# Kernel tuning notes

Hardware: AMD Instinct MI355X
Metric: run time of the kernel (lower is better)

## Reference

```python
import jax, jax.numpy as jnp
import numpy as np

NUM_HEADS = 32
NUM_KV_HEADS = 8
HEAD_DIM = 128
HIDDEN = 4096
ROPE_THETA = 10000.0
RMS_EPS = 1e-6


def setup_inputs() -> dict:
    key = jax.random.key(0)
    k1, k2, k3 = jax.random.split(key, 3)
    T = 2048
    qkv_out = (NUM_HEADS + 2 * NUM_KV_HEADS) * HEAD_DIM  # 6144
    return {
        "positions": jnp.arange(T, dtype=jnp.int64),
        "hidden_states": jax.random.normal(k1, (T, HIDDEN), dtype=jnp.float32),
        "wqkv": jax.random.normal(k2, (qkv_out, HIDDEN), dtype=jnp.float32) * 0.02,
        "wo": jax.random.normal(k3, (HIDDEN, NUM_HEADS * HEAD_DIM), dtype=jnp.float32) * 0.02,
        "q_norm_w": jnp.ones((HEAD_DIM,), dtype=jnp.float32),
        "k_norm_w": jnp.ones((HEAD_DIM,), dtype=jnp.float32),
    }


def _rms_norm(x, w):
    # per-head RMSNorm over last dim, computed in fp32 (matches Dots1RMSNorm)
    xf = x.astype(jnp.float32)
    var = jnp.mean(xf * xf, axis=-1, keepdims=True)
    return (w * (xf * jax.lax.rsqrt(var + RMS_EPS))).astype(x.dtype)


def _rope(x, positions):
    # NeoX-style rotary: rotate halves. x: [T, H, D]
    half = HEAD_DIM // 2
    inv_freq = 1.0 / (ROPE_THETA ** (jnp.arange(0, half, dtype=jnp.float32) / half))
    ang = positions.astype(jnp.float32)[:, None] * inv_freq  # [T, half]
    cos = jnp.cos(ang)[:, None, :]  # [T,1,half]
    sin = jnp.sin(ang)[:, None, :]
    x1, x2 = x[..., :half], x[..., half:]
    return jnp.concatenate([x1 * cos - x2 * sin, x2 * cos + x1 * sin], axis=-1)


def reference(positions, hidden_states, wqkv, wo, q_norm_w, k_norm_w):
    T = hidden_states.shape[0]
    q_size = NUM_HEADS * HEAD_DIM
    kv_size = NUM_KV_HEADS * HEAD_DIM
    qkv = hidden_states @ wqkv.T  # [T, q_size + 2*kv_size]
    q = qkv[:, :q_size].reshape(T, NUM_HEADS, HEAD_DIM)
    k = qkv[:, q_size:q_size + kv_size].reshape(T, NUM_KV_HEADS, HEAD_DIM)
    v = qkv[:, q_size + kv_size:].reshape(T, NUM_KV_HEADS, HEAD_DIM)

    q = _rms_norm(q, q_norm_w)
    k = _rms_norm(k, k_norm_w)
    q = _rope(q, positions)
    k = _rope(k, positions)

    # GQA: expand kv heads to query heads (group of 4)
    group = NUM_HEADS // NUM_KV_HEADS
    k = jnp.repeat(k, group, axis=1)  # [T, H, D]
    v = jnp.repeat(v, group, axis=1)

    scale = HEAD_DIM ** -0.5
    scores = jnp.einsum('thd,shd->hts', q, k) * scale  # [H, T, T]
    causal = positions[:, None] >= positions[None, :]
    scores = jnp.where(causal[None, :, :], scores, jnp.finfo(scores.dtype).min)
    probs = jax.nn.softmax(scores, axis=-1)
    attn = jnp.einsum('hts,shd->thd', probs, v)  # [T, H, D]
    out = attn.reshape(T, NUM_HEADS * HEAD_DIM) @ wo.T  # [T, HIDDEN]
    return out
```

## Files before the change

kernel.cpp:

```cpp
#include <hip/hip_runtime.h>


#define T_SEQ 2048
#define HID   4096
#define NH    32
#define NKVH  8
#define HD    128
#define QKVN  6144
#define QSZ   4096
#define KVSZ  1024

typedef unsigned short u16;
typedef __attribute__((ext_vector_type(8))) short short8;
typedef __attribute__((ext_vector_type(4))) float floatx4;

__device__ __forceinline__ float bf2f(u16 u) {
  union { unsigned int i; float f; } c; c.i = ((unsigned int)u) << 16; return c.f;
}
__device__ __forceinline__ u16 f2bf(float f) {
  union { float f; unsigned int i; } c; c.f = f;
  unsigned int u = c.i;
  return (u16)((u + 0x7FFFu + ((u >> 16) & 1u)) >> 16);
}
__device__ __forceinline__ floatx4 mfma16(short8 a, short8 b, floatx4 c) {
  return __builtin_amdgcn_mfma_f32_16x16x32_bf16(a, b, c, 0, 0, 0);
}

#define GLD16(g, l) __builtin_amdgcn_global_load_lds( \
    (__attribute__((address_space(1))) unsigned int*)(g), \
    (__attribute__((address_space(3))) unsigned int*)(l), 16, 0, 0)

__global__ __launch_bounds__(256) void cvt_kernel(const float* __restrict__ src,
                                                  u16* __restrict__ dst, int n4) {
  int i = blockIdx.x * 256 + threadIdx.x;
  int stride = gridDim.x * 256;
  for (; i < n4; i += stride) {
    float4 v = ((const float4*)src)[i];
    ushort4 o;
    o.x = f2bf(v.x); o.y = f2bf(v.y); o.z = f2bf(v.z); o.w = f2bf(v.w);
    ((ushort4*)dst)[i] = o;
  }
}

template <int OUT_BF16>
__global__ __launch_bounds__(256, 2) void gemm_bt(const u16* __restrict__ A,
    const u16* __restrict__ B, void* __restrict__ Cv, int M, int N, int K) {
  __shared__ __attribute__((aligned(16))) u16 As[128 * 32];
  __shared__ __attribute__((aligned(16))) u16 Bs[128 * 32];
  const int tid = threadIdx.x;
  const int wave = tid >> 6, lane = tid & 63;
  const int lq = lane >> 4, lc = lane & 15;
  const int wm = wave >> 1, wn = wave & 1;
  const int m0 = blockIdx.y * 128, n0 = blockIdx.x * 128;

  floatx4 acc[4][4];
#pragma unroll
  for (int i = 0; i < 4; ++i)
#pragma unroll
    for (int j = 0; j < 4; ++j) acc[i][j] = {0.f, 0.f, 0.f, 0.f};

  int achunk[4], bchunk[4];
#pragma unroll
  for (int i = 0; i < 4; ++i) {
    int ml = wm * 64 + i * 16 + lc;
    achunk[i] = ml * 4 + (lq ^ ((ml >> 1) & 3));
    int nl = wn * 64 + i * 16 + lc;
    bchunk[i] = nl * 4 + (lq ^ ((nl >> 1) & 3));
  }

  for (int k0 = 0; k0 < K; k0 += 32) {
#pragma unroll
    for (int r = 0; r < 2; ++r) {
      int L = r * 256 + tid;
      int mm = L >> 2;
      int cc = (L & 3) ^ ((mm >> 1) & 3);
      GLD16(A + (size_t)(m0 + mm) * K + k0 + cc * 8,
            As + (size_t)(r * 256 + wave * 64) * 8);
      GLD16(B + (size_t)(n0 + mm) * K + k0 + cc * 8,
            Bs + (size_t)(r * 256 + wave * 64) * 8);
    }
    __syncthreads();
    short8 af[4], bfr[4];
#pragma unroll
    for (int mi = 0; mi < 4; ++mi) af[mi] = *(const short8*)&As[achunk[mi] * 8];
#pragma unroll
    for (int ni = 0; ni < 4; ++ni) bfr[ni] = *(const short8*)&Bs[bchunk[ni] * 8];
#pragma unroll
    for (int mi = 0; mi < 4; ++mi)
#pragma unroll
      for (int ni = 0; ni < 4; ++ni)
        acc[mi][ni] = mfma16(af[mi], bfr[ni], acc[mi][ni]);
    __syncthreads();
  }
#pragma unroll
  for (int mi = 0; mi < 4; ++mi) {
    int row = m0 + wm * 64 + mi * 16 + lq * 4;
#pragma unroll
    for (int ni = 0; ni < 4; ++ni) {
      int col = n0 + wn * 64 + ni * 16 + lc;
#pragma unroll
      for (int r = 0; r < 4; ++r) {
        if (OUT_BF16)
          ((u16*)Cv)[(size_t)(row + r) * N + col] = f2bf(acc[mi][ni][r]);
        else
          ((float*)Cv)[(size_t)(row + r) * N + col] = acc[mi][ni][r];
      }
    }
  }
}

__global__ __launch_bounds__(256) void norm_rope_kernel(const u16* __restrict__ qkv,
    const float* __restrict__ qw, const float* __restrict__ kw,
    u16* __restrict__ Qo, u16* __restrict__ Ko) {
  const int t = blockIdx.x;
  const int hs = blockIdx.y * 4 + (threadIdx.x >> 6);
  const int l = threadIdx.x & 63;
  const bool isq = hs < NH;
  const int col0 = isq ? hs * HD : QSZ + (hs - NH) * HD;
  const u16* src = qkv + (size_t)t * QKVN + col0;
  float x1 = bf2f(src[l]);
  float x2 = bf2f(src[l + 64]);
  float ss = x1 * x1 + x2 * x2;
#pragma unroll
  for (int m = 1; m < 64; m <<= 1) ss += __shfl_xor(ss, m);
  float rstd = rsqrtf(ss * (1.0f / HD) + 1e-6f);
  const float* w = isq ? qw : kw;
  float n1 = x1 * rstd * w[l];
  float n2 = x2 * rstd * w[l + 64];
  float inv = exp2f((float)l * -0.20762050593045158f);
  float ang = (float)t * inv;
  float s, c;
  __sincosf(ang, &s, &c);
  float o1 = n1 * c - n2 * s;
  float o2 = n2 * c + n1 * s;
  if (isq) {
    o1 *= 0.08838834764831845f; o2 *= 0.08838834764831845f;
    u16* dst = Qo + ((size_t)hs * T_SEQ + t) * HD;
    dst[l] = f2bf(o1); dst[l + 64] = f2bf(o2);
  } else {
    u16* dst = Ko + ((size_t)(hs - NH) * T_SEQ + t) * HD;
    dst[l] = f2bf(o1); dst[l + 64] = f2bf(o2);
  }
}

__global__ __launch_bounds__(256) void vtrans_kernel(const u16* __restrict__ qkv,
                                                     u16* __restrict__ VT) {
  __shared__ u16 lds[128][65];
  const int h = blockIdx.y;
  const int t0 = blockIdx.x * 64;
  const int tid = threadIdx.x;
#pragma unroll 4
  for (int i = 0; i < 32; ++i) {
    int f = i * 256 + tid;
    int tl = f >> 7, d = f & 127;
    lds[d][tl] = qkv[(size_t)(t0 + tl) * QKVN + QSZ + KVSZ + h * HD + d];
  }
  __syncthreads();
#pragma unroll 4
  for (int i = 0; i < 32; ++i) {
    int f = i * 256 + tid;
    int d = f >> 6, tl = f & 63;
    VT[((size_t)h * HD + d) * T_SEQ + t0 + tl] = lds[d][tl];
  }
}

__global__ __launch_bounds__(256, 2) void attn_kernel(const u16* __restrict__ Qg,
    const u16* __restrict__ Kg, const u16* __restrict__ VTg, u16* __restrict__ Og) {
  __shared__ __attribute__((aligned(16))) u16 Ks[8192];
  __shared__ __attribute__((aligned(16))) u16 Vs[2][8192];
  __shared__ __attribute__((aligned(16))) u16 Ps[8192];

  const int bid = blockIdx.x;
  const int h = bid & 31;
  const int qq = bid >> 5;
  const int qt = (qq < 8) ? (15 - qq) : (qq - 8);
  const int kvh = h >> 2;
  const int tid = threadIdx.x;
  const int wave = tid >> 6, lane = tid & 63;
  const int lq = lane >> 4, lc = lane & 15;

  const u16* kbase[4];
  const u16* vbase[4];
#pragma unroll
  for (int i = 0; i < 4; ++i) {
    int L = i * 256 + tid;
    int s = L >> 4, cp = L & 15;
    kbase[i] = Kg + ((size_t)kvh * T_SEQ + s) * HD + ((cp ^ (s & 15)) * 8);
    int d = L >> 3, cv = L & 7;
    vbase[i] = VTg + ((size_t)kvh * HD + d) * T_SEQ + ((cv ^ (d & 7)) * 8);
  }

  short8 qf[2][4];
#pragma unroll
  for (int mb = 0; mb < 2; ++mb)
#pragma unroll
    for (int ks = 0; ks < 4; ++ks) {
      int t = qt * 128 + wave * 32 + mb * 16 + lc;
      qf[mb][ks] = *(const short8*)&Qg[((size_t)h * T_SEQ + t) * HD + ks * 32 + lq * 8];
    }

  short8 ones;
#pragma unroll
  for (int j = 0; j < 8; ++j) ones[j] = (short)0x3F80;

  floatx4 of[2][8];
  floatx4 lacc[2];
#pragma unroll
  for (int mb = 0; mb < 2; ++mb) {
    lacc[mb] = {0.f, 0.f, 0.f, 0.f};
#pragma unroll
    for (int db = 0; db < 8; ++db) of[mb][db] = {0.f, 0.f, 0.f, 0.f};
  }

  const int ktmax = 2 * qt + 1;
  const int t0g = qt * 128 + wave * 32;
  const int wave_tmax = t0g + 31;

#pragma unroll
  for (int i = 0; i < 4; ++i) {
    GLD16(kbase[i], Ks + (i * 256 + wave * 64) * 8);
    GLD16(vbase[i], Vs[0] + (i * 256 + wave * 64) * 8);
  }

  for (int kt = 0; kt <= ktmax; ++kt) {
    __syncthreads();
    if (kt + 1 <= ktmax) {
      u16* vd = Vs[(kt + 1) & 1] + (size_t)wave * 64 * 8;
#pragma unroll
      for (int i = 0; i < 4; ++i)
        GLD16(vbase[i] + (kt + 1) * 64, vd + i * 256 * 8);
    }
    const bool active = (kt * 64) <= wave_tmax;
    if (active) {
      floatx4 sf[2][4];
#pragma unroll
      for (int mb = 0; mb < 2; ++mb)
#pragma unroll
        for (int nb = 0; nb < 4; ++nb) sf[mb][nb] = {0.f, 0.f, 0.f, 0.f};
#pragma unroll
      for (int ks = 0; ks < 4; ++ks) {
        short8 kf[4];
#pragma unroll
        for (int nb = 0; nb < 4; ++nb)
          kf[nb] = *(const short8*)&Ks[(nb * 16 + lc) * 128 + ((4 * ks + lq) ^ lc) * 8];
#pragma unroll
        for (int mb = 0; mb < 2; ++mb)
#pragma unroll
          for (int nb = 0; nb < 4; ++nb)
            sf[mb][nb] = mfma16(kf[nb], qf[mb][ks], sf[mb][nb]);
      }
      const bool nm = (kt * 64 + 63) > t0g;
#pragma unroll
      for (int mb = 0; mb < 2; ++mb) {
        const int trow = wave * 32 + mb * 16 + lc;
        const int tg = qt * 128 + trow;
#pragma unroll
        for (int nb = 0; nb < 4; ++nb) {
          ushort4 u;
          float p0 = __expf(sf[mb][nb][0]);
          float p1 = __expf(sf[mb][nb][1]);
          float p2 = __expf(sf[mb][nb][2]);
          float p3 = __expf(sf[mb][nb][3]);
          if (nm) {
            int sg = kt * 64 + nb * 16 + lq * 4;
            p0 = (sg + 0 <= tg) ? p0 : 0.f;
            p1 = (sg + 1 <= tg) ? p1 : 0.f;
            p2 = (sg + 2 <= tg) ? p2 : 0.f;
            p3 = (sg + 3 <= tg) ? p3 : 0.f;
          }
          u.x = f2bf(p0); u.y = f2bf(p1); u.z = f2bf(p2); u.w = f2bf(p3);
          int c = 2 * nb + (lq >> 1);
          *(ushort4*)&Ps[trow * 64 + ((c ^ (trow & 7)) * 8) + (lq & 1) * 4] = u;
        }
      }
    }
    __syncthreads();
    if (kt + 1 <= ktmax) {
      u16* kd = Ks + (size_t)wave * 64 * 8;
#pragma unroll
      for (int i = 0; i < 4; ++i)
        GLD16(kbase[i] + (size_t)(kt + 1) * 8192, kd + i * 256 * 8);
    }
    if (active) {
      const u16* vb = Vs[kt & 1];
      short8 pf[2][2];
#pragma unroll
      for (int mb = 0; mb < 2; ++mb)
#pragma unroll
        for (int k2 = 0; k2 < 2; ++k2) {
          int trow = wave * 32 + mb * 16 + lc;
          pf[mb][k2] =
              *(const short8*)&Ps[trow * 64 + (((4 * k2 + lq) ^ (lc & 7)) * 8)];
        }
#pragma unroll
      for (int k2 = 0; k2 < 2; ++k2) {
#pragma unroll
        for (int db = 0; db < 8; ++db) {
          short8 vf =
              *(const short8*)&vb[(db * 16 + lc) * 64 + (((4 * k2 + lq) ^ (lc & 7)) * 8)];
          of[0][db] = mfma16(pf[0][k2], vf, of[0][db]);
          of[1][db] = mfma16(pf[1][k2], vf, of[1][db]);
        }
        lacc[0] = mfma16(pf[0][k2], ones, lacc[0]);
        lacc[1] = mfma16(pf[1][k2], ones, lacc[1]);
      }
    }
  }
#pragma unroll
  for (int mb = 0; mb < 2; ++mb)
#pragma unroll
    for (int r = 0; r < 4; ++r) {
      float inv = 1.f / lacc[mb][r];
      int tg = qt * 128 + wave * 32 + mb * 16 + lq * 4 + r;
#pragma unroll
      for (int db = 0; db < 8; ++db)
        Og[(size_t)tg * QSZ + h * HD + db * 16 + lc] = f2bf(of[mb][db][r] * inv);
    }
}

extern "C" void kernel_launch(void* const* d_in, const int* in_sizes, int n_in,
                              void* d_out, int out_size, void* d_ws, size_t ws_size,
                              hipStream_t stream) {
  (void)in_sizes; (void)n_in; (void)out_size; (void)ws_size;
  const float* hidden = (const float*)d_in[1];
  const float* wqkv   = (const float*)d_in[2];
  const float* wo     = (const float*)d_in[3];
  const float* qw     = (const float*)d_in[4];
  const float* kw     = (const float*)d_in[5];
  float* out = (float*)d_out;
  char* ws = (char*)d_ws;

  u16* h_bf    = (u16*)(ws + 0);
  u16* wq_bf   = (u16*)(ws + 16777216);
  u16* wo_bf   = (u16*)(ws + 67108864);
  u16* qkv_bf  = (u16*)(ws + 100663296);
  u16* q_bf    = (u16*)(ws + 16777216);
  u16* k_bf    = (u16*)(ws + 33554432);
  u16* vT_bf   = (u16*)(ws + 37748736);
  u16* attn_bf = (u16*)(ws + 0);

  cvt_kernel<<<2048, 256, 0, stream>>>(hidden, h_bf, T_SEQ * HID / 4);
  cvt_kernel<<<4096, 256, 0, stream>>>(wqkv, wq_bf, QKVN * HID / 4);
  cvt_kernel<<<4096, 256, 0, stream>>>(wo, wo_bf, HID * QSZ / 4);

  gemm_bt<1><<<dim3(QKVN / 128, T_SEQ / 128), 256, 0, stream>>>(
      h_bf, wq_bf, qkv_bf, T_SEQ, QKVN, HID);

  norm_rope_kernel<<<dim3(T_SEQ, 10), 256, 0, stream>>>(
      qkv_bf, qw, kw, q_bf, k_bf);
  vtrans_kernel<<<dim3(T_SEQ / 64, NKVH), 256, 0, stream>>>(qkv_bf, vT_bf);

  attn_kernel<<<512, 256, 0, stream>>>(q_bf, k_bf, vT_bf, attn_bf);

  gemm_bt<0><<<dim3(QSZ / 128, T_SEQ / 128), 256, 0, stream>>>(
      attn_bf, wo_bf, out, T_SEQ, QSZ, HID);
}
```

Before: 510.2 us.

## Fuse fp32-to-bf16 conversions, widen GEMM K-tile, and write V transposed from GEMM

The three conversion launches become one kernel that walks all three buffers in a single grid. The GEMM K-tile grows from 32 to 64 with an 8-way XOR swizzle. Blocks are linearized so M tiles vary fastest, which improves reuse of B tiles. The QKV GEMM epilogue writes V columns straight into the transposed VT layout, so the separate transpose kernel and the V part of the intermediate buffer go away. The cost is doubled LDS per block and strided 8-byte stores for the VT output.

```diff
diff --git a/kernel.cpp b/kernel.cpp
--- a/kernel.cpp
+++ b/kernel.cpp
@@ -8,7 +8,7 @@
 #define HD    128
 #define QKVN  6144
 #define QSZ   4096
-#define KVSZ  1024
+#define QKN   5120
 
 typedef unsigned short u16;
 typedef __attribute__((ext_vector_type(8))) short short8;
@@ -30,28 +30,36 @@
     (__attribute__((address_space(1))) unsigned int*)(g), \
     (__attribute__((address_space(3))) unsigned int*)(l), 16, 0, 0)
 
-__global__ __launch_bounds__(256) void cvt_kernel(const float* __restrict__ src,
-                                                  u16* __restrict__ dst, int n4) {
-  int i = blockIdx.x * 256 + threadIdx.x;
+__global__ __launch_bounds__(256) void cvt3_kernel(
+    const float* __restrict__ s0, const float* __restrict__ s1,
+    const float* __restrict__ s2, u16* __restrict__ d0, u16* __restrict__ d1,
+    u16* __restrict__ d2, int n0, int n1, int n2) {
+  int total = n0 + n1 + n2;
   int stride = gridDim.x * 256;
-  for (; i < n4; i += stride) {
-    float4 v = ((const float4*)src)[i];
+  for (int i = blockIdx.x * 256 + threadIdx.x; i < total; i += stride) {
+    const float* s; u16* d; int j = i;
+    if (j < n0)           { s = s0; d = d0; }
+    else if (j < n0 + n1) { j -= n0; s = s1; d = d1; }
+    else                  { j -= n0 + n1; s = s2; d = d2; }
+    float4 v = ((const float4*)s)[j];
     ushort4 o;
     o.x = f2bf(v.x); o.y = f2bf(v.y); o.z = f2bf(v.z); o.w = f2bf(v.w);
-    ((ushort4*)dst)[i] = o;
-  }
-}
-
-template <int OUT_BF16>
+    ((ushort4*)d)[j] = o;
+  }
+}
+
+template <int MODE>
 __global__ __launch_bounds__(256, 2) void gemm_bt(const u16* __restrict__ A,
-    const u16* __restrict__ B, void* __restrict__ Cv, int M, int N, int K) {
-  __shared__ __attribute__((aligned(16))) u16 As[128 * 32];
-  __shared__ __attribute__((aligned(16))) u16 Bs[128 * 32];
+    const u16* __restrict__ B, void* __restrict__ Cv, u16* __restrict__ VT,
+    int mtiles, int K, int ldC) {
+  __shared__ __attribute__((aligned(16))) u16 As[128 * 64];
+  __shared__ __attribute__((aligned(16))) u16 Bs[128 * 64];
   const int tid = threadIdx.x;
   const int wave = tid >> 6, lane = tid & 63;
   const int lq = lane >> 4, lc = lane & 15;
   const int wm = wave >> 1, wn = wave & 1;
-  const int m0 = blockIdx.y * 128, n0 = blockIdx.x * 128;
+  const int by = blockIdx.x % mtiles, bx = blockIdx.x / mtiles;
+  const int m0 = by * 128, n0 = bx * 128;
 
   floatx4 acc[4][4];
 #pragma unroll
@@ -59,57 +67,81 @@
 #pragma unroll
     for (int j = 0; j < 4; ++j) acc[i][j] = {0.f, 0.f, 0.f, 0.f};
 
-  int achunk[4], bchunk[4];
+  int arow[4], brow[4];
 #pragma unroll
   for (int i = 0; i < 4; ++i) {
-    int ml = wm * 64 + i * 16 + lc;
-    achunk[i] = ml * 4 + (lq ^ ((ml >> 1) & 3));
-    int nl = wn * 64 + i * 16 + lc;
-    bchunk[i] = nl * 4 + (lq ^ ((nl >> 1) & 3));
-  }
-
-  for (int k0 = 0; k0 < K; k0 += 32) {
-#pragma unroll
-    for (int r = 0; r < 2; ++r) {
-      int L = r * 256 + tid;
-      int mm = L >> 2;
-      int cc = (L & 3) ^ ((mm >> 1) & 3);
-      GLD16(A + (size_t)(m0 + mm) * K + k0 + cc * 8,
-            As + (size_t)(r * 256 + wave * 64) * 8);
-      GLD16(B + (size_t)(n0 + mm) * K + k0 + cc * 8,
-            Bs + (size_t)(r * 256 + wave * 64) * 8);
+    arow[i] = wm * 64 + i * 16 + lc;
+    brow[i] = wn * 64 + i * 16 + lc;
+  }
+
+  const u16* asrc[4]; const u16* bsrc[4];
+#pragma unroll
+  for (int r = 0; r < 4; ++r) {
+    int L = r * 256 + tid;
+    int mm = L >> 3;
+    int cc = (L & 7) ^ (mm & 7);
+    asrc[r] = A + (size_t)(m0 + mm) * K + cc * 8;
+    bsrc[r] = B + (size_t)(n0 + mm) * K + cc * 8;
+  }
+
+  for (int k0 = 0; k0 < K; k0 += 64) {
+#pragma unroll
+    for (int r = 0; r < 4; ++r) {
+      GLD16(asrc[r] + k0, As + (r * 256 + wave * 64) * 8);
+      GLD16(bsrc[r] + k0, Bs + (r * 256 + wave * 64) * 8);
     }
     __syncthreads();
-    short8 af[4], bfr[4];
-#pragma unroll
-    for (int mi = 0; mi < 4; ++mi) af[mi] = *(const short8*)&As[achunk[mi] * 8];
-#pragma unroll
-    for (int ni = 0; ni < 4; ++ni) bfr[ni] = *(const short8*)&Bs[bchunk[ni] * 8];
-#pragma unroll
-    for (int mi = 0; mi < 4; ++mi)
+#pragma unroll
+    for (int kb = 0; kb < 2; ++kb) {
+      short8 af[4], bfr[4];
+#pragma unroll
+      for (int mi = 0; mi < 4; ++mi)
+        af[mi] = *(const short8*)&As[arow[mi] * 64 + (((kb * 4 + lq) ^ (arow[mi] & 7)) * 8)];
 #pragma unroll
       for (int ni = 0; ni < 4; ++ni)
-        acc[mi][ni] = mfma16(af[mi], bfr[ni], acc[mi][ni]);
+        bfr[ni] = *(const short8*)&Bs[brow[ni] * 64 + (((kb * 4 + lq) ^ (brow[ni] & 7)) * 8)];
+#pragma unroll
+      for (int mi = 0; mi < 4; ++mi)
+#pragma unroll
+        for (int ni = 0; ni < 4; ++ni)
+          acc[mi][ni] = mfma16(af[mi], bfr[ni], acc[mi][ni]);
+    }
     __syncthreads();
   }
-#pragma unroll
-  for (int mi = 0; mi < 4; ++mi) {
-    int row = m0 + wm * 64 + mi * 16 + lq * 4;
-#pragma unroll
-    for (int ni = 0; ni < 4; ++ni) {
-      int col = n0 + wn * 64 + ni * 16 + lc;
-#pragma unroll
-      for (int r = 0; r < 4; ++r) {
-        if (OUT_BF16)
-          ((u16*)Cv)[(size_t)(row + r) * N + col] = f2bf(acc[mi][ni][r]);
-        else
-          ((float*)Cv)[(size_t)(row + r) * N + col] = acc[mi][ni][r];
-      }
-    }
-  }
-}
-
-__global__ __launch_bounds__(256) void norm_rope_kernel(const u16* __restrict__ qkv,
+
+  if (MODE == 1 && n0 >= 5120) {
+#pragma unroll
+    for (int mi = 0; mi < 4; ++mi) {
+      int row = m0 + wm * 64 + mi * 16 + lq * 4;
+#pragma unroll
+      for (int ni = 0; ni < 4; ++ni) {
+        int rel = n0 + wn * 64 + ni * 16 + lc - 5120;
+        ushort4 u;
+        u.x = f2bf(acc[mi][ni][0]); u.y = f2bf(acc[mi][ni][1]);
+        u.z = f2bf(acc[mi][ni][2]); u.w = f2bf(acc[mi][ni][3]);
+        *(ushort4*)&VT[(size_t)rel * T_SEQ + row] = u;
+      }
+    }
+  } else {
+#pragma unroll
+    for (int mi = 0; mi < 4; ++mi) {
+      int row = m0 + wm * 64 + mi * 16 + lq * 4;
+#pragma unroll
+      for (int ni = 0; ni < 4; ++ni) {
+        int col = n0 + wn * 64 + ni * 16 + lc;
+#pragma unroll
+        for (int r = 0; r < 4; ++r) {
+          if (MODE == 1)
+            ((u16*)Cv)[(size_t)(row + r) * ldC + col] = f2bf(acc[mi][ni][r]);
+          else
+            ((float*)Cv)[(size_t)(row + r) * ldC + col] = acc[mi][ni][r];
+        }
+      }
+    }
+  }
+}
+
+__global__ __launch_bounds__(256) void norm_rope_kernel(const u16* __restrict__ qk,
     const float* __restrict__ qw, const float* __restrict__ kw,
     u16* __restrict__ Qo, u16* __restrict__ Ko) {
   const int t = blockIdx.x;
@@ -117,7 +149,7 @@
   const int l = threadIdx.x & 63;
   const bool isq = hs < NH;
   const int col0 = isq ? hs * HD : QSZ + (hs - NH) * HD;
-  const u16* src = qkv + (size_t)t * QKVN + col0;
+  const u16* src = qk + (size_t)t * QKN + col0;
   float x1 = bf2f(src[l]);
   float x2 = bf2f(src[l + 64]);
   float ss = x1 * x1 + x2 * x2;
@@ -143,27 +175,6 @@
   }
 }
 
-__global__ __launch_bounds__(256) void vtrans_kernel(const u16* __restrict__ qkv,
-                                                     u16* __restrict__ VT) {
-  __shared__ u16 lds[128][65];
-  const int h = blockIdx.y;
-  const int t0 = blockIdx.x * 64;
-  const int tid = threadIdx.x;
-#pragma unroll 4
-  for (int i = 0; i < 32; ++i) {
-    int f = i * 256 + tid;
-    int tl = f >> 7, d = f & 127;
-    lds[d][tl] = qkv[(size_t)(t0 + tl) * QKVN + QSZ + KVSZ + h * HD + d];
-  }
-  __syncthreads();
-#pragma unroll 4
-  for (int i = 0; i < 32; ++i) {
-    int f = i * 256 + tid;
-    int d = f >> 6, tl = f & 63;
-    VT[((size_t)h * HD + d) * T_SEQ + t0 + tl] = lds[d][tl];
-  }
-}
-
 __global__ __launch_bounds__(256, 2) void attn_kernel(const u16* __restrict__ Qg,
     const u16* __restrict__ Kg, const u16* __restrict__ VTg, u16* __restrict__ Og) {
   __shared__ __attribute__((aligned(16))) u16 Ks[8192];
@@ -333,25 +344,24 @@
   u16* h_bf    = (u16*)(ws + 0);
   u16* wq_bf   = (u16*)(ws + 16777216);
   u16* wo_bf   = (u16*)(ws + 67108864);
-  u16* qkv_bf  = (u16*)(ws + 100663296);
+  u16* vT_bf   = (u16*)(ws + 100663296);
+  u16* qk_bf   = (u16*)(ws + 104857600);
   u16* q_bf    = (u16*)(ws + 16777216);
   u16* k_bf    = (u16*)(ws + 33554432);
-  u16* vT_bf   = (u16*)(ws + 37748736);
   u16* attn_bf = (u16*)(ws + 0);
 
-  cvt_kernel<<<2048, 256, 0, stream>>>(hidden, h_bf, T_SEQ * HID / 4);
-  cvt_kernel<<<4096, 256, 0, stream>>>(wqkv, wq_bf, QKVN * HID / 4);
-  cvt_kernel<<<4096, 256, 0, stream>>>(wo, wo_bf, HID * QSZ / 4);
-
-  gemm_bt<1><<<dim3(QKVN / 128, T_SEQ / 128), 256, 0, stream>>>(
-      h_bf, wq_bf, qkv_bf, T_SEQ, QKVN, HID);
+  cvt3_kernel<<<8192, 256, 0, stream>>>(
+      hidden, wqkv, wo, h_bf, wq_bf, wo_bf,
+      T_SEQ * HID / 4, QKVN * HID / 4, HID * QSZ / 4);
+
+  gemm_bt<1><<<768, 256, 0, stream>>>(h_bf, wq_bf, qk_bf, vT_bf,
+                                      T_SEQ / 128, HID, QKN);
 
   norm_rope_kernel<<<dim3(T_SEQ, 10), 256, 0, stream>>>(
-      qkv_bf, qw, kw, q_bf, k_bf);
-  vtrans_kernel<<<dim3(T_SEQ / 64, NKVH), 256, 0, stream>>>(qkv_bf, vT_bf);
+      qk_bf, qw, kw, q_bf, k_bf);
 
   attn_kernel<<<512, 256, 0, stream>>>(q_bf, k_bf, vT_bf, attn_bf);
 
-  gemm_bt<0><<<dim3(QSZ / 128, T_SEQ / 128), 256, 0, stream>>>(
-      attn_bf, wo_bf, out, T_SEQ, QSZ, HID);
-}
+  gemm_bt<0><<<512, 256, 0, stream>>>(attn_bf, wo_bf, out, vT_bf,
+                                      T_SEQ / 128, HID, QSZ);
+}
```

Measured after the change: 486.5 us. 1.05x faster.
